# Kernel optimization log

Hardware: AMD Instinct MI355X
Metric: run time of the kernel (lower is better)

Reference implementation:

```python
import jax, jax.numpy as jnp
import numpy as np

N_LAYER = 6
EPS = 1e-5
TWO_PI = 2.0 * np.pi
THETA = 2.0 ** 16


def _ln(x):
    # LayerNorm over last dim, no affine (elementwise_affine=False)
    m = jnp.mean(x, axis=-1, keepdims=True)
    v = jnp.mean((x - m) ** 2, axis=-1, keepdims=True)
    return (x - m) / jnp.sqrt(v + EPS)


def _rope_tables(T, N):
    t = jnp.arange(N, dtype=jnp.float32)
    q = jnp.floor(t / 2.0) * 2.0  # quantize(t, 2)
    freqs = 1.0 / (THETA ** (q / N)) / TWO_PI  # [N]
    pos = jnp.arange(T, dtype=jnp.float32)
    angles = (pos[:, None] * freqs[None, :] % 1.0) * TWO_PI  # [T, N]
    return jnp.cos(angles), jnp.sin(angles)


def _rotate_half(v):
    # stack((-v_odd, v_even), -1).view(shape): interleaved rotation
    return jnp.stack((-v[..., 1::2], v[..., ::2]), axis=-1).reshape(v.shape)


def setup_inputs() -> dict:
    key = jax.random.key(0)
    ks = jax.random.split(key, 6)
    B, T = 1, 512
    D, nh, mult, vocab = 256, 4, 128, 256
    N = mult * D // nh  # 8192
    idx = jax.random.randint(ks[0], (B, T), 0, vocab)
    std = 0.02
    embed = jax.random.normal(ks[1], (vocab, D), jnp.float32) * std
    encoder = jax.random.normal(ks[2], (nh, D, N), jnp.float32) * std
    encoder_v = jax.random.normal(ks[3], (nh, D, N), jnp.float32) * std
    decoder = jax.random.normal(ks[4], (nh * N, D), jnp.float32) * std
    lm_head = jax.random.normal(ks[5], (D, vocab), jnp.float32) * std
    return {"idx": idx, "embed": embed, "encoder": encoder,
            "encoder_v": encoder_v, "decoder": decoder, "lm_head": lm_head}


def reference(idx, embed, encoder, encoder_v, decoder, lm_head):
    B, T = idx.shape
    nh, D, N = encoder.shape
    cos, sin = _rope_tables(T, N)  # [T, N]
    causal = jnp.tril(jnp.ones((T, T), dtype=bool), k=-1)  # strict lower

    x = _ln(embed[idx])  # [B, T, D]
    for _ in range(N_LAYER):  # single shared layer applied n_layer times
        x_sparse = jax.nn.relu(jnp.einsum('btd,hdn->bhtn', x, encoder))
        qr = x_sparse * cos + _rotate_half(x_sparse) * sin  # RoPE on Q=K
        scores = jnp.einsum('bhtn,bhsn->bhts', qr, qr)
        scores = jnp.where(causal, scores, 0.0)  # tril(diagonal=-1), no softmax
        yKV = _ln(jnp.einsum('bhts,bsd->bhtd', scores, x))  # V = x broadcast over heads
        y_sparse = jax.nn.relu(jnp.einsum('bhtd,hdn->bhtn', yKV, encoder_v))
        xy = x_sparse * y_sparse  # [B, nh, T, N]
        xy = xy.transpose(0, 2, 1, 3).reshape(B, T, nh * N)
        y = _ln(xy @ decoder)  # [B, T, D]
        x = _ln(x + y)
    logits = x @ lm_head  # [B, T, vocab]
    return logits
```

## Files before the change

kernel.cpp:

```cpp
#include <hip/hip_runtime.h>
#include <hip/hip_bf16.h>

#define T   512
#define D   256
#define H   4
#define NN  8192
#define V   256
#define EPSF 1e-5f
#define QKS 4
#define DSPLIT 16
#define N_LAYER 6

typedef __bf16 bf16;
typedef __attribute__((__ext_vector_type__(8))) __bf16 bf16x8;
typedef __attribute__((__ext_vector_type__(4))) __bf16 bf16x4;
typedef __attribute__((__ext_vector_type__(4))) float  f32x4;

#define MFMA16(a, b, c) __builtin_amdgcn_mfma_f32_16x16x32_bf16((a), (b), (c), 0, 0, 0)
#define GLD16(g, l)                                                         \
    __builtin_amdgcn_global_load_lds(                                       \
        (const __attribute__((address_space(1))) void*)(g),                 \
        (__attribute__((address_space(3))) void*)(l), 16, 0, 0)

__device__ __forceinline__ float blk_sum256(float v, float* red) {
#pragma unroll
    for (int off = 32; off > 0; off >>= 1) v += __shfl_down(v, off, 64);
    int lane = threadIdx.x & 63, w = threadIdx.x >> 6;
    __syncthreads();
    if (lane == 0) red[w] = v;
    __syncthreads();
    return red[0] + red[1] + red[2] + red[3];
}

__global__ __launch_bounds__(256) void tcvt_k(const float* __restrict__ in,
                                              bf16* __restrict__ out, int R, int C) {
    __shared__ float t[32][33];
    size_t hoff = (size_t)blockIdx.z * R * C;
    int c0 = blockIdx.x * 32, r0 = blockIdx.y * 32;
    int x = threadIdx.x & 31, y = threadIdx.x >> 5;
#pragma unroll
    for (int p = 0; p < 4; ++p)
        t[y + 8 * p][x] = in[hoff + (size_t)(r0 + y + 8 * p) * C + c0 + x];
    __syncthreads();
#pragma unroll
    for (int p = 0; p < 4; ++p)
        out[hoff + (size_t)(c0 + y + 8 * p) * R + r0 + x] = (bf16)t[x][y + 8 * p];
}

__global__ __launch_bounds__(256) void rope_tab_k(bf16* __restrict__ cosH,
                                                  bf16* __restrict__ sinH) {
    int k = blockIdx.x * 256 + threadIdx.x;
    int t = blockIdx.y;
    float q = (float)(2 * k);
    float f = exp2f(q * (-16.0f / (float)NN)) * 0.15915494309189535f;
    float u = fmodf((float)t * f, 1.0f);
    float a = u * 6.283185307179586f;
    cosH[(size_t)t * (NN / 2) + k] = (bf16)cosf(a);
    sinH[(size_t)t * (NN / 2) + k] = (bf16)sinf(a);
}

__global__ __launch_bounds__(256) void embed_ln_k(const int* __restrict__ idx,
                                                  const float* __restrict__ embed,
                                                  float* __restrict__ x,
                                                  bf16* __restrict__ xb,
                                                  bf16* __restrict__ xbT) {
    __shared__ float red[4];
    int t = blockIdx.x, d = threadIdx.x;
    float e = embed[(size_t)idx[t] * D + d];
    float m = blk_sum256(e, red) * (1.0f / D);
    float df = e - m;
    float vv = blk_sum256(df * df, red) * (1.0f / D);
    float r = df * rsqrtf(vv + EPSF);
    x[(size_t)t * D + d] = r;
    xb[(size_t)t * D + d] = (bf16)r;
    xbT[(size_t)d * T + t] = (bf16)r;
}

__device__ __forceinline__ void gemm_core64(const bf16* __restrict__ Ap, size_t lda,
                                            const bf16* __restrict__ Bp, size_t ldb,
                                            int ksteps, bf16* lds,
                                            f32x4 acc[2][2], int tid) {
    int lane = tid & 63, wid = tid >> 6;
    int wr = (wid >> 1) * 32, wc = (wid & 1) * 32;
    int fr = lane & 15, s = lane >> 4;
    int srow = wid * 16 + (lane >> 3);
    int sx   = ((lane & 7) ^ (srow & 7)) * 8;
    const bf16* ag = Ap + (size_t)srow * lda + sx;
    const bf16* bg = Bp + (size_t)srow * ldb + sx;
    bf16* a_w = lds + wid * 1024;
    bf16* b_w = lds + 8192 + wid * 1024;
    int ar = wr + fr, br = wc + fr;
    int aoff0 = ar * 128 + (((s)     ^ (ar & 7)) << 4);
    int aoff1 = ar * 128 + (((4 + s) ^ (ar & 7)) << 4);
    int boff0 = br * 128 + (((s)     ^ (br & 7)) << 4);
    int boff1 = br * 128 + (((4 + s) ^ (br & 7)) << 4);
    GLD16(ag, a_w);  GLD16(ag + 8 * lda, a_w + 512);
    GLD16(bg, b_w);  GLD16(bg + 8 * ldb, b_w + 512);
    __syncthreads();
    for (int ks = 0; ks < ksteps; ++ks) {
        int cur = ks & 1;
        if (ks + 1 < ksteps) {
            int nxt = cur ^ 1;
            size_t ko = (size_t)(ks + 1) * 64;
            bf16* an = lds + nxt * 4096 + wid * 1024;
            bf16* bn = lds + 8192 + nxt * 4096 + wid * 1024;
            GLD16(ag + ko, an);  GLD16(ag + ko + 8 * lda, an + 512);
            GLD16(bg + ko, bn);  GLD16(bg + ko + 8 * ldb, bn + 512);
        }
        const char* cA = (const char*)(lds + cur * 4096);
        const char* cB = (const char*)(lds + 8192 + cur * 4096);
        bf16x8 a00 = *(const bf16x8*)(cA + aoff0);
        bf16x8 a01 = *(const bf16x8*)(cA + aoff1);
        bf16x8 a10 = *(const bf16x8*)(cA + aoff0 + 2048);
        bf16x8 a11 = *(const bf16x8*)(cA + aoff1 + 2048);
        bf16x8 b00 = *(const bf16x8*)(cB + boff0);
        bf16x8 b01 = *(const bf16x8*)(cB + boff1);
        bf16x8 b10 = *(const bf16x8*)(cB + boff0 + 2048);
        bf16x8 b11 = *(const bf16x8*)(cB + boff1 + 2048);
        acc[0][0] = MFMA16(a00, b00, acc[0][0]);
        acc[0][0] = MFMA16(a01, b01, acc[0][0]);
        acc[0][1] = MFMA16(a00, b10, acc[0][1]);
        acc[0][1] = MFMA16(a01, b11, acc[0][1]);
        acc[1][0] = MFMA16(a10, b00, acc[1][0]);
        acc[1][0] = MFMA16(a11, b01, acc[1][0]);
        acc[1][1] = MFMA16(a10, b10, acc[1][1]);
        acc[1][1] = MFMA16(a11, b11, acc[1][1]);
        __syncthreads();
    }
}

template <int MODE>
__global__ __launch_bounds__(256) void enc_mfma_k(const bf16* __restrict__ A,
                                                  const bf16* __restrict__ Wt,
                                                  bf16* __restrict__ xs,
                                                  bf16* __restrict__ qr,
                                                  const bf16* __restrict__ cosH,
                                                  const bf16* __restrict__ sinH,
                                                  int aHeadStride) {
    __shared__ __align__(16) char smem[32768];
    bf16 (*Ot)[76] = (bf16(*)[76])smem;
    bf16 (*Or)[76] = (bf16(*)[76])(smem + 9728);
    int h = blockIdx.z;
    int row0 = blockIdx.y * 64, col0 = blockIdx.x * 64;
    const bf16* Ap = A + (size_t)h * aHeadStride + (size_t)row0 * D;
    const bf16* Bp = Wt + ((size_t)h * NN + col0) * D;
    int tid = threadIdx.x;
    f32x4 acc[2][2];
#pragma unroll
    for (int i = 0; i < 2; ++i)
#pragma unroll
        for (int j = 0; j < 2; ++j) acc[i][j] = f32x4{0.f, 0.f, 0.f, 0.f};
    gemm_core64(Ap, D, Bp, D, D / 64, (bf16*)smem, acc, tid);

    int lane = tid & 63, wid = tid >> 6;
    int wr = (wid >> 1) * 32, wc = (wid & 1) * 32;
    int fr = lane & 15, fq = lane >> 4;
    float vv[2][2][4];
#pragma unroll
    for (int mi = 0; mi < 2; ++mi)
#pragma unroll
        for (int ni = 0; ni < 2; ++ni)
#pragma unroll
            for (int j = 0; j < 4; ++j)
                vv[mi][ni][j] = fmaxf((float)acc[mi][ni][j], 0.0f);

#pragma unroll
    for (int mi = 0; mi < 2; ++mi)
#pragma unroll
        for (int ni = 0; ni < 2; ++ni)
#pragma unroll
            for (int j = 0; j < 4; ++j) {
                int lr = wr + mi * 16 + fq * 4 + j;
                int lc = wc + ni * 16 + fr;
                float v = vv[mi][ni][j];
                Ot[lr][lc] = (bf16)v;
                if (MODE == 0) {
                    float p = __shfl_xor(v, 1, 64);
                    int m = row0 + lr;
                    int n = col0 + lc;
                    float cs = (float)cosH[(size_t)m * (NN / 2) + (n >> 1)];
                    float sn = (float)sinH[(size_t)m * (NN / 2) + (n >> 1)];
                    Or[lr][lc] = (bf16)(v * cs + ((n & 1) ? p * sn : -p * sn));
                }
            }
    __syncthreads();
    int er = tid >> 2, ec = (tid & 3) * 16;
    size_t gbase = ((size_t)h * T + row0 + er) * NN + col0 + ec;
    bf16x8 o0 = *(bf16x8*)&Ot[er][ec];
    bf16x8 o1 = *(bf16x8*)&Ot[er][ec + 8];

    if (MODE == 0) {
        bf16x8 q0 = *(bf16x8*)&Or[er][ec];
        bf16x8 q1 = *(bf16x8*)&Or[er][ec + 8];
        *(bf16x8*)(xs + gbase) = o0;
        *(bf16x8*)(xs + gbase + 8) = o1;
        *(bf16x8*)(qr + gbase) = q0;
        *(bf16x8*)(qr + gbase + 8) = q1;
    } else {
        bf16x8 x0 = *(const bf16x8*)(xs + gbase);
        bf16x8 x1 = *(const bf16x8*)(xs + gbase + 8);
        bf16x8 r0v, r1v;
#pragma unroll
        for (int k = 0; k < 8; ++k) {
            r0v[k] = (bf16)((float)o0[k] * (float)x0[k]);
            r1v[k] = (bf16)((float)o1[k] * (float)x1[k]);
        }
        *(bf16x8*)(xs + gbase) = r0v;
        *(bf16x8*)(xs + gbase + 8) = r1v;
    }
}

__global__ __launch_bounds__(256) void qq_mfma_k(const bf16* __restrict__ qrb,
                                                 bf16* __restrict__ spartb) {
    __shared__ __align__(16) char smem[32768];
    int g = blockIdx.x & 15;
    int h = g >> 2, ksplit = g & 3;
    int p = blockIdx.x >> 4;
    int ti = 0, accu = 0;
    while (accu + ti + 1 <= p) { ++ti; accu += ti; }
    int tj = p - accu;
    const bf16* Q = qrb + (size_t)h * T * NN + (size_t)ksplit * (NN / QKS);
    const bf16* Ap = Q + (size_t)(ti * 64) * NN;
    const bf16* Bp = Q + (size_t)(tj * 64) * NN;
    int tid = threadIdx.x;
    f32x4 acc[2][2];
#pragma unroll
    for (int i = 0; i < 2; ++i)
#pragma unroll
        for (int j = 0; j < 2; ++j) acc[i][j] = f32x4{0.f, 0.f, 0.f, 0.f};
    gemm_core64(Ap, NN, Bp, NN, (NN / QKS) / 64, (bf16*)smem, acc, tid);

    int lane = tid & 63, wid = tid >> 6;
    int wr = (wid >> 1) * 32, wc = (wid & 1) * 32;
    int fr = lane & 15, fq = lane >> 4;
    bf16* outp = spartb + (size_t)(ksplit * H + h) * T * T;
#pragma unroll
    for (int mi = 0; mi < 2; ++mi)
#pragma unroll
        for (int ni = 0; ni < 2; ++ni) {
            int s = tj * 64 + wc + ni * 16 + fr;
            int mbase = ti * 64 + wr + mi * 16 + fq * 4;
#pragma unroll
            for (int j = 0; j < 4; ++j)
                outp[(size_t)(mbase + j) * T + s] = (bf16)acc[mi][ni][j];
        }
}

__global__ __launch_bounds__(256) void mask_cvt_k(const bf16* __restrict__ spartb,
                                                  bf16* __restrict__ sb) {
    int t = blockIdx.x * 2 + (threadIdx.x >> 7);
    int h = blockIdx.y;
    int l = threadIdx.x & 127;
    int s = l * 4;
    const bf16* s0 = spartb + ((size_t)h * T + t) * T + s;
    const size_t st = (size_t)H * T * T;
    float a0 = 0, a1 = 0, a2 = 0, a3 = 0;
#pragma unroll
    for (int k = 0; k < QKS; ++k) {
        bf16x4 w = *(const bf16x4*)(s0 + k * st);
        a0 += (float)w[0]; a1 += (float)w[1]; a2 += (float)w[2]; a3 += (float)w[3];
    }
    bf16x4 o;
    o[0] = (bf16)((s + 0 < t) ? a0 : 0.0f);
    o[1] = (bf16)((s + 1 < t) ? a1 : 0.0f);
    o[2] = (bf16)((s + 2 < t) ? a2 : 0.0f);
    o[3] = (bf16)((s + 3 < t) ? a3 : 0.0f);
    *(bf16x4*)(sb + ((size_t)h * T + t) * T + s) = o;
}

__global__ __launch_bounds__(256) void av_mfma_k(const bf16* __restrict__ sb,
                                                 const bf16* __restrict__ xbT,
                                                 float* __restrict__ ykv_pre) {
    __shared__ __align__(16) char smem[32768];
    int h = blockIdx.z;
    int ti = blockIdx.y;
    int row0 = ti * 64, col0 = blockIdx.x * 64;
    const bf16* Ap = sb + ((size_t)h * T + row0) * T;
    const bf16* Bp = xbT + (size_t)col0 * T;
    int tid = threadIdx.x;
    f32x4 acc[2][2];
#pragma unroll
    for (int i = 0; i < 2; ++i)
#pragma unroll
        for (int j = 0; j < 2; ++j) acc[i][j] = f32x4{0.f, 0.f, 0.f, 0.f};
    gemm_core64(Ap, T, Bp, T, ti + 1, (bf16*)smem, acc, tid);

    int lane = tid & 63, wid = tid >> 6;
    int wr = (wid >> 1) * 32, wc = (wid & 1) * 32;
    int fr = lane & 15, fq = lane >> 4;
#pragma unroll
    for (int mi = 0; mi < 2; ++mi)
#pragma unroll
        for (int ni = 0; ni < 2; ++ni) {
            int n = col0 + wc + ni * 16 + fr;
            int mbase = row0 + wr + mi * 16 + fq * 4;
#pragma unroll
            for (int j = 0; j < 4; ++j)
                ykv_pre[((size_t)h * T + (mbase + j)) * D + n] = acc[mi][ni][j];
        }
}

__global__ __launch_bounds__(256) void ykv_ln_k(const float* __restrict__ ykv_pre,
                                                bf16* __restrict__ ykvb) {
    __shared__ float red[4];
    int t = blockIdx.x, h = blockIdx.y, d = threadIdx.x;
    float a = ykv_pre[((size_t)h * T + t) * D + d];
    float m = blk_sum256(a, red) * (1.0f / D);
    float df = a - m;
    float vv = blk_sum256(df * df, red) * (1.0f / D);
    ykvb[((size_t)h * T + t) * D + d] = (bf16)(df * rsqrtf(vv + EPSF));
}

__global__ __launch_bounds__(256) void dec_mfma_k(const bf16* __restrict__ xyb,
                                                  const bf16* __restrict__ decT,
                                                  float* __restrict__ ypart) {
    __shared__ __align__(16) char smem[32768];
    int ks = blockIdx.x & 15;
    int t  = blockIdx.x >> 4;
    int col0 = (t & 3) * 64, row0 = (t >> 2) * 64;
    int cbeg = ks * ((H * NN) / DSPLIT);
    int h = cbeg >> 13, n0 = cbeg & (NN - 1);
    const bf16* Ap = xyb + ((size_t)h * T + row0) * NN + n0;
    const bf16* Bp = decT + (size_t)col0 * (H * NN) + cbeg;
    int tid = threadIdx.x;
    f32x4 acc[2][2];
#pragma unroll
    for (int i = 0; i < 2; ++i)
#pragma unroll
        for (int j = 0; j < 2; ++j) acc[i][j] = f32x4{0.f, 0.f, 0.f, 0.f};
    gemm_core64(Ap, NN, Bp, H * NN, (H * NN / DSPLIT) / 64, (bf16*)smem, acc, tid);

    int lane = tid & 63, wid = tid >> 6;
    int wr = (wid >> 1) * 32, wc = (wid & 1) * 32;
    int fr = lane & 15, fq = lane >> 4;
#pragma unroll
    for (int mi = 0; mi < 2; ++mi)
#pragma unroll
        for (int ni = 0; ni < 2; ++ni) {
            int n = col0 + wc + ni * 16 + fr;
            int mbase = row0 + wr + mi * 16 + fq * 4;
#pragma unroll
            for (int j = 0; j < 4; ++j)
                ypart[((size_t)ks * T + (mbase + j)) * D + n] = acc[mi][ni][j];
        }
}

__global__ __launch_bounds__(256) void final_ln_k(const float* __restrict__ ypart,
                                                  float* __restrict__ x,
                                                  bf16* __restrict__ xb,
                                                  bf16* __restrict__ xbT) {
    __shared__ float red[4];
    int t = blockIdx.x, d = threadIdx.x;
    float ys = 0.0f;
#pragma unroll
    for (int ks = 0; ks < DSPLIT; ++ks) ys += ypart[((size_t)ks * T + t) * D + d];
    float m = blk_sum256(ys, red) * (1.0f / D);
    float df = ys - m;
    float vv = blk_sum256(df * df, red) * (1.0f / D);
    float yln = df * rsqrtf(vv + EPSF);
    float val = x[(size_t)t * D + d] + yln;
    float m2 = blk_sum256(val, red) * (1.0f / D);
    float df2 = val - m2;
    float v2 = blk_sum256(df2 * df2, red) * (1.0f / D);
    float r = df2 * rsqrtf(v2 + EPSF);
    x[(size_t)t * D + d] = r;
    xb[(size_t)t * D + d] = (bf16)r;
    xbT[(size_t)d * T + t] = (bf16)r;
}

__global__ __launch_bounds__(256) void logits_k(const float* __restrict__ x,
                                                const float* __restrict__ lm,
                                                float* __restrict__ out) {
    int t = blockIdx.x, v = threadIdx.x;
    float a = 0.0f;
    for (int d = 0; d < D; ++d)
        a = fmaf(x[(size_t)t * D + d], lm[(size_t)d * V + v], a);
    out[(size_t)t * V + v] = a;
}

extern "C" void kernel_launch(void* const* d_in, const int* in_sizes, int n_in,
                              void* d_out, int out_size, void* d_ws, size_t ws_size,
                              hipStream_t stream) {
    const int*   idx       = (const int*)d_in[0];
    const float* embed     = (const float*)d_in[1];
    const float* encoder   = (const float*)d_in[2];
    const float* encoder_v = (const float*)d_in[3];
    const float* decoder   = (const float*)d_in[4];
    const float* lm_head   = (const float*)d_in[5];
    float* out = (float*)d_out;

    char* W = (char*)d_ws;
    float* x       = (float*)W; W += (size_t)T * D * 4;
    float* scratch = (float*)W; W += (size_t)QKS * H * T * T * 4;
    bf16* xb    = (bf16*)W; W += (size_t)T * D * 2;
    bf16* xbT   = (bf16*)W; W += (size_t)D * T * 2;
    bf16* sb    = (bf16*)W; W += (size_t)H * T * T * 2;
    bf16* ykvb  = (bf16*)W; W += (size_t)H * T * D * 2;
    bf16* encT  = (bf16*)W; W += (size_t)H * NN * D * 2;
    bf16* encVT = (bf16*)W; W += (size_t)H * NN * D * 2;
    bf16* decT  = (bf16*)W; W += (size_t)D * H * NN * 2;
    bf16* cosH  = (bf16*)W; W += (size_t)T * (NN / 2) * 2;
    bf16* sinH  = (bf16*)W; W += (size_t)T * (NN / 2) * 2;
    bf16* xs    = (bf16*)W; W += (size_t)H * T * NN * 2;
    bf16* qr    = (bf16*)W; W += (size_t)H * T * NN * 2;
    bf16* spartb = (bf16*)scratch;

    tcvt_k<<<dim3(NN / 32, D / 32, H), 256, 0, stream>>>(encoder, encT, D, NN);
    tcvt_k<<<dim3(NN / 32, D / 32, H), 256, 0, stream>>>(encoder_v, encVT, D, NN);
    tcvt_k<<<dim3(D / 32, (H * NN) / 32, 1), 256, 0, stream>>>(decoder, decT, H * NN, D);
    rope_tab_k<<<dim3((NN / 2) / 256, T), 256, 0, stream>>>(cosH, sinH);

    embed_ln_k<<<T, 256, 0, stream>>>(idx, embed, x, xb, xbT);

    for (int layer = 0; layer < N_LAYER; ++layer) {
        enc_mfma_k<0><<<dim3(NN / 64, T / 64, H), 256, 0, stream>>>(
            xb, encT, xs, qr, cosH, sinH, 0);
        qq_mfma_k<<<576, 256, 0, stream>>>(qr, spartb);
        mask_cvt_k<<<dim3(T / 2, H), 256, 0, stream>>>(spartb, sb);
        av_mfma_k<<<dim3(D / 64, T / 64, H), 256, 0, stream>>>(sb, xbT, scratch);
        ykv_ln_k<<<dim3(T, H), 256, 0, stream>>>(scratch, ykvb);
        enc_mfma_k<1><<<dim3(NN / 64, T / 64, H), 256, 0, stream>>>(
            ykvb, encVT, xs, nullptr, nullptr, nullptr, T * D);
        dec_mfma_k<<<512, 256, 0, stream>>>(xs, decT, scratch);
        final_ln_k<<<T, 256, 0, stream>>>(scratch, x, xb, xbT);
    }

    logits_k<<<T, 256, 0, stream>>>(x, lm_head, out);
}
```

Measured before the change: 690.0 us.

## Enlarge encoder GEMM tiles to 128x128 and drop LDS-staged epilogue

Adds a 128x128 double-buffered MFMA GEMM core with an XOR-swizzled LDS layout, and switches both encoder kernels to it, cutting the grid by 4x. Each wave now computes a 64x64 sub-tile with 16 accumulators, which raises operand reuse per LDS load. The epilogue no longer stages results in shared memory for vectorized 16-byte stores; it writes scalar bf16 values straight to global memory. This trades coalesced wide stores for simpler code, adds register pressure, and leaves fewer blocks to fill the CUs.

```diff
diff --git a/kernel.cpp b/kernel.cpp
--- a/kernel.cpp
+++ b/kernel.cpp
@@ -129,6 +129,62 @@
     }
 }
 
+__device__ __forceinline__ void gemm_core128v2(const bf16* __restrict__ Ap, size_t lda,
+                                               const bf16* __restrict__ Bp, size_t ldb,
+                                               int ksteps, bf16* lds,
+                                               f32x4 acc[4][4], int tid) {
+    int lane = tid & 63, wid = tid >> 6;
+    int wr = (wid >> 1) * 64, wc = (wid & 1) * 64;
+    int fr = lane & 15, s = lane >> 4;
+    int srow = wid * 16 + (lane >> 3);
+    int sx   = ((lane & 7) ^ (srow & 7)) * 8;
+    const bf16* ag = Ap + (size_t)srow * lda + sx;
+    const bf16* bg = Bp + (size_t)srow * ldb + sx;
+    bf16* a_w = lds + wid * 1024;
+    bf16* b_w = lds + 16384 + wid * 1024;
+    int ar = wr + fr, br = wc + fr;
+    int aoff0 = (ar & 63) * 128 + (((s)     ^ (fr & 7)) << 4) + (wr >> 6) * 8192;
+    int aoff1 = (ar & 63) * 128 + (((4 + s) ^ (fr & 7)) << 4) + (wr >> 6) * 8192;
+    int boff0 = (br & 63) * 128 + (((s)     ^ (fr & 7)) << 4) + (wc >> 6) * 8192;
+    int boff1 = (br & 63) * 128 + (((4 + s) ^ (fr & 7)) << 4) + (wc >> 6) * 8192;
+    GLD16(ag, a_w);                 GLD16(ag + 8 * lda, a_w + 512);
+    GLD16(ag + 64 * lda, a_w + 4096); GLD16(ag + 72 * lda, a_w + 4608);
+    GLD16(bg, b_w);                 GLD16(bg + 8 * ldb, b_w + 512);
+    GLD16(bg + 64 * ldb, b_w + 4096); GLD16(bg + 72 * ldb, b_w + 4608);
+    __syncthreads();
+    for (int ks = 0; ks < ksteps; ++ks) {
+        int cur = ks & 1;
+        if (ks + 1 < ksteps) {
+            int nxt = cur ^ 1;
+            size_t ko = (size_t)(ks + 1) * 64;
+            bf16* an = lds + nxt * 8192 + wid * 1024;
+            bf16* bn = lds + 16384 + nxt * 8192 + wid * 1024;
+            GLD16(ag + ko, an);                 GLD16(ag + ko + 8 * lda, an + 512);
+            GLD16(ag + ko + 64 * lda, an + 4096); GLD16(ag + ko + 72 * lda, an + 4608);
+            GLD16(bg + ko, bn);                 GLD16(bg + ko + 8 * ldb, bn + 512);
+            GLD16(bg + ko + 64 * ldb, bn + 4096); GLD16(bg + ko + 72 * ldb, bn + 4608);
+        }
+        const char* cA = (const char*)(lds + cur * 8192);
+        const char* cB = (const char*)(lds + 16384 + cur * 8192);
+        bf16x8 a0[4], a1[4], b0[4], b1[4];
+#pragma unroll
+        for (int i = 0; i < 4; ++i) {
+            a0[i] = *(const bf16x8*)(cA + aoff0 + i * 2048);
+            a1[i] = *(const bf16x8*)(cA + aoff1 + i * 2048);
+            b0[i] = *(const bf16x8*)(cB + boff0 + i * 2048);
+            b1[i] = *(const bf16x8*)(cB + boff1 + i * 2048);
+        }
+#pragma unroll
+        for (int i = 0; i < 4; ++i)
+#pragma unroll
+            for (int j = 0; j < 4; ++j) {
+                acc[i][j] = MFMA16(a0[i], b0[j], acc[i][j]);
+                acc[i][j] = MFMA16(a1[i], b1[j], acc[i][j]);
+            }
+        __syncthreads();
+    }
+}
+
 template <int MODE>
 __global__ __launch_bounds__(256) void enc_mfma_k(const bf16* __restrict__ A,
                                                   const bf16* __restrict__ Wt,
@@ -137,77 +193,44 @@
                                                   const bf16* __restrict__ cosH,
                                                   const bf16* __restrict__ sinH,
                                                   int aHeadStride) {
-    __shared__ __align__(16) char smem[32768];
-    bf16 (*Ot)[76] = (bf16(*)[76])smem;
-    bf16 (*Or)[76] = (bf16(*)[76])(smem + 9728);
+    __shared__ __align__(16) bf16 smem[32768];
     int h = blockIdx.z;
-    int row0 = blockIdx.y * 64, col0 = blockIdx.x * 64;
+    int row0 = blockIdx.y * 128, col0 = blockIdx.x * 128;
     const bf16* Ap = A + (size_t)h * aHeadStride + (size_t)row0 * D;
     const bf16* Bp = Wt + ((size_t)h * NN + col0) * D;
     int tid = threadIdx.x;
-    f32x4 acc[2][2];
-#pragma unroll
-    for (int i = 0; i < 2; ++i)
-#pragma unroll
-        for (int j = 0; j < 2; ++j) acc[i][j] = f32x4{0.f, 0.f, 0.f, 0.f};
-    gemm_core64(Ap, D, Bp, D, D / 64, (bf16*)smem, acc, tid);
-
-    int lane = tid & 63, wid = tid >> 6;
-    int wr = (wid >> 1) * 32, wc = (wid & 1) * 32;
+    f32x4 acc[4][4];
+#pragma unroll
+    for (int i = 0; i < 4; ++i)
+#pragma unroll
+        for (int j = 0; j < 4; ++j) acc[i][j] = f32x4{0.f, 0.f, 0.f, 0.f};
+    gemm_core128v2(Ap, D, Bp, D, D / 64, smem, acc, tid);
+
+    int lane = tid & 63, wid = tid >> 6;
+    int wr = (wid >> 1) * 64, wc = (wid & 1) * 64;
     int fr = lane & 15, fq = lane >> 4;
-    float vv[2][2][4];
-#pragma unroll
-    for (int mi = 0; mi < 2; ++mi)
-#pragma unroll
-        for (int ni = 0; ni < 2; ++ni)
-#pragma unroll
-            for (int j = 0; j < 4; ++j)
-                vv[mi][ni][j] = fmaxf((float)acc[mi][ni][j], 0.0f);
-
-#pragma unroll
-    for (int mi = 0; mi < 2; ++mi)
-#pragma unroll
-        for (int ni = 0; ni < 2; ++ni)
+#pragma unroll
+    for (int mi = 0; mi < 4; ++mi)
+#pragma unroll
+        for (int ni = 0; ni < 4; ++ni)
 #pragma unroll
             for (int j = 0; j < 4; ++j) {
-                int lr = wr + mi * 16 + fq * 4 + j;
-                int lc = wc + ni * 16 + fr;
-                float v = vv[mi][ni][j];
-                Ot[lr][lc] = (bf16)v;
+                int m = row0 + wr + mi * 16 + fq * 4 + j;
+                int n = col0 + wc + ni * 16 + fr;
+                size_t base = ((size_t)h * T + m) * NN + n;
+                float v = fmaxf((float)acc[mi][ni][j], 0.0f);
                 if (MODE == 0) {
                     float p = __shfl_xor(v, 1, 64);
-                    int m = row0 + lr;
-                    int n = col0 + lc;
                     float cs = (float)cosH[(size_t)m * (NN / 2) + (n >> 1)];
                     float sn = (float)sinH[(size_t)m * (NN / 2) + (n >> 1)];
-                    Or[lr][lc] = (bf16)(v * cs + ((n & 1) ? p * sn : -p * sn));
+                    float qv = v * cs + ((n & 1) ? p * sn : -p * sn);
+                    xs[base] = (bf16)v;
+                    qr[base] = (bf16)qv;
+                } else {
+                    float xo = (float)xs[base];
+                    xs[base] = (bf16)(xo * v);
                 }
             }
-    __syncthreads();
-    int er = tid >> 2, ec = (tid & 3) * 16;
-    size_t gbase = ((size_t)h * T + row0 + er) * NN + col0 + ec;
-    bf16x8 o0 = *(bf16x8*)&Ot[er][ec];
-    bf16x8 o1 = *(bf16x8*)&Ot[er][ec + 8];
-
-    if (MODE == 0) {
-        bf16x8 q0 = *(bf16x8*)&Or[er][ec];
-        bf16x8 q1 = *(bf16x8*)&Or[er][ec + 8];
-        *(bf16x8*)(xs + gbase) = o0;
-        *(bf16x8*)(xs + gbase + 8) = o1;
-        *(bf16x8*)(qr + gbase) = q0;
-        *(bf16x8*)(qr + gbase + 8) = q1;
-    } else {
-        bf16x8 x0 = *(const bf16x8*)(xs + gbase);
-        bf16x8 x1 = *(const bf16x8*)(xs + gbase + 8);
-        bf16x8 r0v, r1v;
-#pragma unroll
-        for (int k = 0; k < 8; ++k) {
-            r0v[k] = (bf16)((float)o0[k] * (float)x0[k]);
-            r1v[k] = (bf16)((float)o1[k] * (float)x1[k]);
-        }
-        *(bf16x8*)(xs + gbase) = r0v;
-        *(bf16x8*)(xs + gbase + 8) = r1v;
-    }
 }
 
 __global__ __launch_bounds__(256) void qq_mfma_k(const bf16* __restrict__ qrb,
@@ -413,13 +436,13 @@
     embed_ln_k<<<T, 256, 0, stream>>>(idx, embed, x, xb, xbT);
 
     for (int layer = 0; layer < N_LAYER; ++layer) {
-        enc_mfma_k<0><<<dim3(NN / 64, T / 64, H), 256, 0, stream>>>(
+        enc_mfma_k<0><<<dim3(NN / 128, T / 128, H), 256, 0, stream>>>(
             xb, encT, xs, qr, cosH, sinH, 0);
         qq_mfma_k<<<576, 256, 0, stream>>>(qr, spartb);
         mask_cvt_k<<<dim3(T / 2, H), 256, 0, stream>>>(spartb, sb);
         av_mfma_k<<<dim3(D / 64, T / 64, H), 256, 0, stream>>>(sb, xbT, scratch);
         ykv_ln_k<<<dim3(T, H), 256, 0, stream>>>(scratch, ykvb);
-        enc_mfma_k<1><<<dim3(NN / 64, T / 64, H), 256, 0, stream>>>(
+        enc_mfma_k<1><<<dim3(NN / 128, T / 128, H), 256, 0, stream>>>(
             ykvb, encVT, xs, nullptr, nullptr, nullptr, T * D);
         dec_mfma_k<<<512, 256, 0, stream>>>(xs, decT, scratch);
         final_ln_k<<<T, 256, 0, stream>>>(scratch, x, xb, xbT);
```

Result: faster. 644.0 us (-6.7%).
